# Optimization experiments

Hardware: AMD Instinct MI355X
Metric: run time of the kernel (lower is better)

## Reference

```python
import jax, jax.numpy as jnp
import numpy as np

B = 8
N = 2048            # max_seq_len
NUM_BUCKETS = 128


def _bucketize(x):
    # floor(log2(clamp(|x|, min=1))) -- canonical log-bucketing of timespans
    xa = jnp.maximum(jnp.abs(x), 1).astype(jnp.float32)
    return jnp.floor(jnp.log(xa) / jnp.log(2.0)).astype(jnp.int32)


def setup_inputs() -> dict:
    key = jax.random.key(0)
    k1, k2, k3 = jax.random.split(key, 3)
    all_timestamps = jnp.sort(
        jax.random.randint(k1, (B, N), 0, 10_000_000, dtype=jnp.int64), axis=1
    )
    ts_w = 0.02 * jax.random.normal(k2, (NUM_BUCKETS + 1,), dtype=jnp.float32)
    pos_w = 0.02 * jax.random.normal(k3, (2 * N - 1,), dtype=jnp.float32)
    return {"all_timestamps": all_timestamps, "ts_w": ts_w, "pos_w": pos_w}


def reference(all_timestamps, ts_w, pos_w):
    n = N
    # Relative position bias: the pad/repeat/reshape/slice trick in the torch
    # code is exactly pos_w[j - i + N - 1] for output element (i, j).
    idx = jnp.arange(n)
    rel_idx = idx[None, :] - idx[:, None] + (n - 1)   # [N, N] in [0, 2N-2]
    rel_pos_bias = pos_w[rel_idx][None, :, :]          # [1, N, N]

    # Bucketized timestamp bias.
    ext = jnp.concatenate([all_timestamps, all_timestamps[:, n - 1 : n]], axis=1)  # [B, N+1]
    diff = ext[:, 1:, None] - ext[:, None, :-1]        # [B, N, N]
    buckets = jnp.clip(_bucketize(diff), 0, NUM_BUCKETS)
    rel_ts_bias = ts_w[buckets]                        # [B, N, N]

    return rel_pos_bias + rel_ts_bias
```

## Files before the change

kernel.cpp:

```cpp
#include <hip/hip_runtime.h>
#include <hip/hip_bf16.h>

__device__ __forceinline__ float np_logf(float xin) {
  union { float f; unsigned u; } v; v.f = xin;
  int e = (int)(v.u >> 23) - 126;
  v.u = (v.u & 0x007fffffu) | 0x3f000000u;
  float m = v.f;
  if (m < 0.70710678118654752440f) { e -= 1; m = m + m; }
  m = m - 1.0f;
  float p = 7.0376836292e-2f;
  p = fmaf(p, m, -1.1514610310e-1f);
  p = fmaf(p, m,  1.1676998740e-1f);
  p = fmaf(p, m, -1.2420140846e-1f);
  p = fmaf(p, m,  1.4249322787e-1f);
  p = fmaf(p, m, -1.6668057665e-1f);
  p = fmaf(p, m,  2.0000714765e-1f);
  p = fmaf(p, m, -2.4999993993e-1f);
  p = fmaf(p, m,  3.3333331174e-1f);
  float z = m * m;
  float y = (p * m) * z;
  float fe = (float)e;
  y = fmaf(fe, -2.12194440e-4f, y);
  y = fmaf(-0.5f, z, y);
  float r = m + y;
  r = fmaf(fe, 0.693359375f, r);
  return r;
}

__device__ __forceinline__ int chain_bucket(unsigned xa, int NBUCK) {
  float lx = np_logf((float)xa);
  float q = lx / 0.6931471824645996f;
  int bb = (int)floorf(q);
  return min(max(bb, 0), NBUCK);
}

__global__ __launch_bounds__(256) void bias_kernel(
    const int* __restrict__ ts, const float* __restrict__ ts_w,
    const float* __restrict__ pos_w,
    float* __restrict__ out, int N, int NB1) {
  __shared__ float sW[512];
  const int tid = threadIdx.x;
  for (int k = tid; k < NB1 && k < 512; k += 256) sW[k] = ts_w[k];
  __syncthreads();

  const int i = blockIdx.x;
  const int b = blockIdx.y;
  const int NBUCK = NB1 - 1;

  const int* tsrow = ts + (size_t)b * N;
  const int tip1 = tsrow[min(i + 1, N - 1)];
  const float* pw = pos_w + (N - 1 - i);
  float* orow = out + ((size_t)b * N + i) * N;

  const int NT = 256;
  int  tj[8];
  float pj[8];
#pragma unroll
  for (int e = 0; e < 8; ++e) {
    int j = tid + e * NT;
    tj[e] = tsrow[j];
    pj[e] = pw[j];
  }

#pragma unroll
  for (int e = 0; e < 8; ++e) {
    int d = tip1 - tj[e];
    unsigned xa = (unsigned)(d < 0 ? -d : d);
    xa |= (unsigned)(xa == 0);
    int k = 31 - __clz((int)xa);
    unsigned lo = xa - (1u << k);
    unsigned hi = (2u << k) - xa;
    bool near = (lo < 256u) | (hi <= 256u);
    int bb;
    if (__any(near)) {
      bb = chain_bucket(xa, NBUCK);
    } else {
      bb = min(k, NBUCK);
    }
    orow[tid + e * NT] = pj[e] + sW[bb];
  }
}

extern "C" void kernel_launch(void* const* d_in, const int* in_sizes, int n_in,
                              void* d_out, int out_size, void* d_ws, size_t ws_size,
                              hipStream_t stream) {
  int i_ts = 0;
  if (in_sizes[1] > in_sizes[i_ts]) i_ts = 1;
  if (in_sizes[2] > in_sizes[i_ts]) i_ts = 2;
  int i_tsw = 0;
  if (in_sizes[1] < in_sizes[i_tsw]) i_tsw = 1;
  if (in_sizes[2] < in_sizes[i_tsw]) i_tsw = 2;
  int i_pw = 3 - i_ts - i_tsw;

  const int* ts = (const int*)d_in[i_ts];
  const float* ts_w = (const float*)d_in[i_tsw];
  const float* pos_w = (const float*)d_in[i_pw];

  const int NB1 = in_sizes[i_tsw];
  const int N = (in_sizes[i_pw] + 1) / 2;
  const int B = in_sizes[i_ts] / N;

  dim3 grid(N, B);
  bias_kernel<<<grid, 256, 0, stream>>>(ts, ts_w, pos_w,
                                        (float*)d_out, N, NB1);
}
```

Baseline: 28.01 us.

## Process eight rows per block, staging pos_w window and timestamps in LDS/registers

Each block now computes eight consecutive output rows instead of one. The timestamp row is loaded once into registers and a sliding window of pos_w is staged in shared memory and reused across the rows. This cuts redundant global loads and per-block setup, at the cost of fewer blocks, extra LDS use, and hardcoded MAXN/ROWS assumptions. The sW buffer also shrinks to 160 entries.

```diff
diff --git a/kernel.cpp b/kernel.cpp
--- a/kernel.cpp
+++ b/kernel.cpp
@@ -1,5 +1,8 @@
 #include <hip/hip_runtime.h>
 #include <hip/hip_bf16.h>
+
+#define MAXN 2048
+#define ROWS 8
 
 __device__ __forceinline__ float np_logf(float xin) {
   union { float f; unsigned u; } v; v.f = xin;
@@ -38,46 +41,48 @@
     const int* __restrict__ ts, const float* __restrict__ ts_w,
     const float* __restrict__ pos_w,
     float* __restrict__ out, int N, int NB1) {
-  __shared__ float sW[512];
+  __shared__ float sW[160];
+  __shared__ float pw_lds[MAXN + ROWS - 1];
   const int tid = threadIdx.x;
-  for (int k = tid; k < NB1 && k < 512; k += 256) sW[k] = ts_w[k];
-  __syncthreads();
-
-  const int i = blockIdx.x;
+  const int i0 = blockIdx.x * ROWS;
   const int b = blockIdx.y;
   const int NBUCK = NB1 - 1;
 
+  for (int k = tid; k < NB1; k += 256) sW[k] = ts_w[k];
+  const int base = N - ROWS - i0;
+  const int plen = N + ROWS - 1;
+  for (int t = tid; t < plen; t += 256) pw_lds[t] = pos_w[base + t];
+  __syncthreads();
+
   const int* tsrow = ts + (size_t)b * N;
-  const int tip1 = tsrow[min(i + 1, N - 1)];
-  const float* pw = pos_w + (N - 1 - i);
-  float* orow = out + ((size_t)b * N + i) * N;
+  int tj[MAXN / 256];
+#pragma unroll
+  for (int e = 0; e < MAXN / 256; ++e) tj[e] = tsrow[tid + e * 256];
 
-  const int NT = 256;
-  int  tj[8];
-  float pj[8];
-#pragma unroll
-  for (int e = 0; e < 8; ++e) {
-    int j = tid + e * NT;
-    tj[e] = tsrow[j];
-    pj[e] = pw[j];
-  }
+  for (int r = 0; r < ROWS; ++r) {
+    const int i = i0 + r;
+    const int tip1 = tsrow[min(i + 1, N - 1)];
+    float* orow = out + ((size_t)b * N + i) * N;
+    const float* pr = pw_lds + (ROWS - 1 - r);
 
 #pragma unroll
-  for (int e = 0; e < 8; ++e) {
-    int d = tip1 - tj[e];
-    unsigned xa = (unsigned)(d < 0 ? -d : d);
-    xa |= (unsigned)(xa == 0);
-    int k = 31 - __clz((int)xa);
-    unsigned lo = xa - (1u << k);
-    unsigned hi = (2u << k) - xa;
-    bool near = (lo < 256u) | (hi <= 256u);
-    int bb;
-    if (__any(near)) {
-      bb = chain_bucket(xa, NBUCK);
-    } else {
-      bb = min(k, NBUCK);
+    for (int e = 0; e < MAXN / 256; ++e) {
+      const int j = tid + e * 256;
+      int d = tip1 - tj[e];
+      unsigned xa = (unsigned)(d < 0 ? -d : d);
+      xa |= (unsigned)(xa == 0);
+      int k = 31 - __clz((int)xa);
+      unsigned lo = xa - (1u << k);
+      unsigned hi = (2u << k) - xa;
+      bool near = (lo < 256u) | (hi <= 256u);
+      int bb;
+      if (__any(near)) {
+        bb = chain_bucket(xa, NBUCK);
+      } else {
+        bb = min(k, NBUCK);
+      }
+      orow[j] = pr[j] + sW[bb];
     }
-    orow[tid + e * NT] = pj[e] + sW[bb];
   }
 }
 
@@ -100,7 +105,7 @@
   const int N = (in_sizes[i_pw] + 1) / 2;
   const int B = in_sizes[i_ts] / N;
 
-  dim3 grid(N, B);
+  dim3 grid(N / ROWS, B);
   bias_kernel<<<grid, 256, 0, stream>>>(ts, ts_w, pos_w,
                                         (float*)d_out, N, NB1);
 }
```

Measured after the change: 30.53 us. +9.0%, slower.
